# Optimization experiments

Hardware: AMD Instinct MI355X
Metric: run time of the kernel (lower is better)

The kernel has to match this reference:

```python
import jax, jax.numpy as jnp
import numpy as np

N_T, N_Y, N_X = 9, 256, 256
DIM_AE = 10
N_B = 16


def _conv(x, w):
    # Conv2d 3x3, stride 1, padding 1, no bias
    return jax.lax.conv_general_dilated(x, w, (1, 1), 'SAME',
                                        dimension_numbers=('NCHW', 'OIHW', 'NCHW'))


def _softplus10(x):
    # F.softplus(x, beta=10)
    return jax.nn.softplus(10.0 * x) / 10.0


def _derivs(u):
    # central finite differences with zero-Dirichlet boundary (dx=dy=1)
    up = jnp.pad(u, ((0, 0), (0, 0), (1, 1), (1, 1)))
    xp, xm = up[..., 2:, 1:-1], up[..., :-2, 1:-1]
    yp, ym = up[..., 1:-1, 2:], up[..., 1:-1, :-2]
    xpyp, xpym = up[..., 2:, 2:], up[..., 2:, :-2]
    xmyp, xmym = up[..., :-2, 2:], up[..., :-2, :-2]
    dx = 0.5 * (xp - xm)
    dy = 0.5 * (yp - ym)
    dxx = xp - 2.0 * u + xm
    dyy = yp - 2.0 * u + ym
    dxy = 0.25 * (xpyp - xpym - xmyp + xmym)
    return dx, dy, dxx, dyy, dxy


def _apply_A(u, kap, m1, m2, h11, h12, h21, h22):
    # SPDE operator: kappa^2 u + m.grad(u) - div(H grad u) (9-point stencil)
    dx, dy, dxx, dyy, dxy = _derivs(u)
    return kap ** 2 * u + m1 * dx + m2 * dy - (h11 * dxx + (h12 + h21) * dxy + h22 * dyy)


def setup_inputs() -> dict:
    key = jax.random.key(0)
    ks = jax.random.split(key, 4)
    x = jax.random.normal(ks[0], (N_B, N_T, N_Y, N_X), jnp.float32)
    kappa = jnp.zeros((1,), jnp.float32)   # overwritten by decoder (diff_only=False)
    m = jnp.zeros((1,), jnp.float32)       # overwritten by decoder
    H = jnp.zeros((N_B, 2, 2, N_Y * N_X, N_T), jnp.float32)  # overwritten by decoder
    def init_w(k, o, i):
        b = 1.0 / np.sqrt(i * 9)
        return jax.random.uniform(k, (o, i, 3, 3), jnp.float32, -b, b)
    w1 = init_w(ks[1], DIM_AE, N_T)
    w2 = init_w(ks[2], 2 * DIM_AE, DIM_AE)
    w3 = init_w(ks[3], 6 * N_T, 2 * DIM_AE)
    return {'x': x, 'kappa': kappa, 'm': m, 'H': H, 'w1': w1, 'w2': w2, 'w3': w3}


def reference(x, kappa, m, H, w1, w2, w3):
    n_b, n_t, n_y, n_x = x.shape
    N = n_y * n_x
    # ---- encoder ----
    p = _conv(jax.nn.relu(x), w1)
    p = _conv(jax.nn.relu(p), w2)
    p = _conv(p, w3)  # (b, 6*n_t, n_y, n_x)
    # ---- decoder ----
    kap = _softplus10(p[:, :n_t])                       # (b,t,y,x)
    md = jnp.stack([p[:, n_t:2 * n_t], p[:, 2 * n_t:3 * n_t]], axis=1)  # (b,2,t,y,x)
    gamma = _softplus10(p[:, 3 * n_t:4 * n_t])
    gflat = jnp.transpose(gamma, (0, 2, 3, 1)).reshape(n_b, N * n_t)    # (y,x,t) order
    vx = jnp.transpose(p[:, 4 * n_t:5 * n_t], (0, 2, 3, 1)).reshape(n_b, N * n_t)
    vy = jnp.transpose(p[:, 5 * n_t:6 * n_t], (0, 2, 3, 1)).reshape(n_b, N * n_t)
    vxy = jnp.stack([vx, vy], axis=2)                   # (b, K, 2)
    Hd = (jnp.einsum('ij,bk->bijk', jnp.eye(2, dtype=x.dtype), gflat)
          + jnp.einsum('bki,bkj->bijk', vxy, vxy))
    kap_d = kap.reshape(n_b, 1, N, n_t)        # literal reshapes as in original
    m_d = md.reshape(n_b, 2, N, n_t)
    H_d = Hd.reshape(n_b, 2, 2, N, n_t)
    # ---- per-timestep fields on (n_x, n_y) grid, node = ix*n_y + iy ----
    def to_grid(f):  # (b, N, t) -> (b, t, n_x, n_y)
        return jnp.transpose(f, (0, 2, 1)).reshape(n_b, n_t, n_x, n_y)
    kg = to_grid(kap_d[:, 0])
    m1g, m2g = to_grid(m_d[:, 0]), to_grid(m_d[:, 1])
    h11, h12 = to_grid(H_d[:, 0, 0]), to_grid(H_d[:, 0, 1])
    h21, h22 = to_grid(H_d[:, 1, 0]), to_grid(H_d[:, 1, 1])
    # ---- block-tridiagonal precision Q applied to x (never materialized) ----
    xg = jnp.transpose(x, (0, 1, 3, 2))  # (b,t,n_x,n_y), matches permute(0,2,1)
    M = lambda u: u + _apply_A(u, kg, m1g, m2g, h11, h12, h21, h22)  # I + dt*A, dt=1
    w = M(xg)   # M_t x_t
    v = M(w)    # M_t M_t x_t
    qx = jnp.concatenate([
        v[:, :1] - w[:, 1:2],
        -w[:, :-2] + v[:, 1:-1] + xg[:, 1:-1] - w[:, 2:],
        -w[:, -2:-1] + v[:, -1:],
    ], axis=1)
    x_out = jnp.sum(xg * qx, axis=(1, 2, 3))  # x^T Q x per batch, (b,)
    kappa_r = kap_d.reshape(n_b, 1, n_x, n_y, n_t)
    m_r = m_d.reshape(n_b, 2, n_x, n_y, n_t)
    H_r = H_d.reshape(n_b, 2, 2, n_x, n_y, n_t)
    return x_out, kappa_r, m_r, H_r
```

## Files before the change

kernel.cpp:

```cpp
#include <hip/hip_runtime.h>
#include <math.h>

#define NB 16
#define NT 9
#define PLANE 65536
#define KAP_B 589824
#define M_B   1179648
#define H_B   2359296

#define OUT_KAP 16
#define OUT_M   9437200
#define OUT_H   28311568

__device__ __forceinline__ float sp10(float x) {
  float z = 10.0f * x;
  return (fmaxf(z, 0.0f) + log1pf(__expf(-fabsf(z)))) * 0.1f;
}

__global__ __launch_bounds__(1024) void transpose_kernel(const float* __restrict__ x,
                                                         float* __restrict__ xg) {
  __shared__ float t_[32][33];
  const int plane = blockIdx.z;
  const float* src = x + (size_t)plane * PLANE;
  float* dst = xg + (size_t)plane * PLANE;
  const int x0 = blockIdx.x * 32, y0 = blockIdx.y * 32;
  t_[threadIdx.y][threadIdx.x] = src[(y0 + threadIdx.y) * 256 + x0 + threadIdx.x];
  __syncthreads();
  dst[(x0 + threadIdx.y) * 256 + (y0 + threadIdx.x)] = t_[threadIdx.x][threadIdx.y];
}

template <int IC, int OC, bool RELU_IN>
__global__ __launch_bounds__(256, 4) void conv2px(const float* __restrict__ in,
                                                  const float* __restrict__ wt,
                                                  float* __restrict__ out) {
  __shared__ float tile[IC][18][35];
  const int b = blockIdx.z;
  const int x0 = blockIdx.x * 32, y0 = blockIdx.y * 16;
  const int tx = threadIdx.x, ty = threadIdx.y;
  const int tid = ty * 16 + tx;
  const float* inb = in + (size_t)b * IC * PLANE;
  for (int idx = tid; idx < IC * 612; idx += 256) {
    int ic = idx / 612;
    int rem = idx - ic * 612;
    int r = rem / 34, c = rem - r * 34;
    int gy = y0 + r - 1, gx = x0 + c - 1;
    float v = 0.f;
    if (gy >= 0 && gy < 256 && gx >= 0 && gx < 256) {
      v = inb[ic * PLANE + gy * 256 + gx];
      if (RELU_IN) v = fmaxf(v, 0.f);
    }
    tile[ic][r][c] = v;
  }
  __syncthreads();
  float acc0[OC], acc1[OC];
#pragma unroll
  for (int oc = 0; oc < OC; ++oc) { acc0[oc] = 0.f; acc1[oc] = 0.f; }
  for (int ic = 0; ic < IC; ++ic) {
    float p[3][4];
#pragma unroll
    for (int r = 0; r < 3; ++r)
#pragma unroll
      for (int c = 0; c < 4; ++c) p[r][c] = tile[ic][ty + r][2 * tx + c];
#pragma unroll
    for (int oc = 0; oc < OC; ++oc) {
      const float* w9 = wt + (oc * IC + ic) * 9;
      acc0[oc] += p[0][0] * w9[0] + p[0][1] * w9[1] + p[0][2] * w9[2]
                + p[1][0] * w9[3] + p[1][1] * w9[4] + p[1][2] * w9[5]
                + p[2][0] * w9[6] + p[2][1] * w9[7] + p[2][2] * w9[8];
      acc1[oc] += p[0][1] * w9[0] + p[0][2] * w9[1] + p[0][3] * w9[2]
                + p[1][1] * w9[3] + p[1][2] * w9[4] + p[1][3] * w9[5]
                + p[2][1] * w9[6] + p[2][2] * w9[7] + p[2][3] * w9[8];
    }
  }
  float* outb = out + (size_t)b * OC * PLANE + (y0 + ty) * 256 + x0 + 2 * tx;
#pragma unroll
  for (int oc = 0; oc < OC; ++oc) {
    float2 v2 = make_float2(acc0[oc], acc1[oc]);
    *reinterpret_cast<float2*>(&outb[oc * PLANE]) = v2;
  }
}

__global__ __launch_bounds__(512, 4) void conv3_fused(const float* __restrict__ in,
                                                      const float* __restrict__ wt,
                                                      float* __restrict__ out_kap,
                                                      float* __restrict__ out_m,
                                                      float* __restrict__ out_H) {
  __shared__ float tile[20][18][35];
  const int b = blockIdx.z;
  const int x0 = blockIdx.x * 32, y0 = blockIdx.y * 16;
  const int tx = threadIdx.x, ty = threadIdx.y;
  const int h = __builtin_amdgcn_readfirstlane((int)threadIdx.z);
  const int tid = (int)threadIdx.z * 256 + ty * 16 + tx;
  const float* inb = in + (size_t)b * 20 * PLANE;
  for (int idx = tid; idx < 20 * 612; idx += 512) {
    int ic = idx / 612;
    int rem = idx - ic * 612;
    int r = rem / 34, c = rem - r * 34;
    int gy = y0 + r - 1, gx = x0 + c - 1;
    float v = 0.f;
    if (gy >= 0 && gy < 256 && gx >= 0 && gx < 256)
      v = inb[ic * PLANE + gy * 256 + gx];
    tile[ic][r][c] = v;
  }
  __syncthreads();
  float acc0[27], acc1[27];
#pragma unroll
  for (int oc = 0; oc < 27; ++oc) { acc0[oc] = 0.f; acc1[oc] = 0.f; }
  const float* wh = wt + (size_t)h * 27 * 20 * 9;
  for (int ic = 0; ic < 20; ++ic) {
    float p[3][4];
#pragma unroll
    for (int r = 0; r < 3; ++r)
#pragma unroll
      for (int c = 0; c < 4; ++c) p[r][c] = tile[ic][ty + r][2 * tx + c];
#pragma unroll
    for (int oc = 0; oc < 27; ++oc) {
      const float* w9 = wh + (oc * 20 + ic) * 9;
      acc0[oc] += p[0][0] * w9[0] + p[0][1] * w9[1] + p[0][2] * w9[2]
                + p[1][0] * w9[3] + p[1][1] * w9[4] + p[1][2] * w9[5]
                + p[2][0] * w9[6] + p[2][1] * w9[7] + p[2][2] * w9[8];
      acc1[oc] += p[0][1] * w9[0] + p[0][2] * w9[1] + p[0][3] * w9[2]
                + p[1][1] * w9[3] + p[1][2] * w9[4] + p[1][3] * w9[5]
                + p[2][1] * w9[6] + p[2][2] * w9[7] + p[2][3] * w9[8];
    }
  }
  const int n0 = (y0 + ty) * 256 + x0 + 2 * tx;
  if (h == 0) {
    float* kapb = out_kap + (size_t)b * KAP_B;
#pragma unroll
    for (int t = 0; t < 9; ++t) {
      float2 v2 = make_float2(sp10(acc0[t]), sp10(acc1[t]));
      *reinterpret_cast<float2*>(&kapb[t * PLANE + n0]) = v2;
    }
    float* mb = out_m + (size_t)b * M_B;
#pragma unroll
    for (int c = 0; c < 18; ++c) {
      float2 v2 = make_float2(acc0[9 + c], acc1[9 + c]);
      *reinterpret_cast<float2*>(&mb[c * PLANE + n0]) = v2;
    }
  } else {
    float* hb0 = out_H + (size_t)b * H_B + (size_t)n0 * 9;
#pragma unroll
    for (int t = 0; t < 9; ++t) {
      float g0 = sp10(acc0[t]), g1 = sp10(acc1[t]);
      float vx0 = acc0[9 + t], vy0 = acc0[18 + t];
      float vx1 = acc1[9 + t], vy1 = acc1[18 + t];
      hb0[t] = g0 + vx0 * vx0;
      hb0[KAP_B + t] = vx0 * vy0;
      hb0[2 * KAP_B + t] = vx0 * vy0;
      hb0[3 * KAP_B + t] = g0 + vy0 * vy0;
      hb0[9 + t] = g1 + vx1 * vx1;
      hb0[KAP_B + 9 + t] = vx1 * vy1;
      hb0[2 * KAP_B + 9 + t] = vx1 * vy1;
      hb0[3 * KAP_B + 9 + t] = g1 + vy1 * vy1;
    }
  }
}

template <bool FINAL>
__global__ __launch_bounds__(256) void m_kernel(const float* __restrict__ u_in,
                                                const float* __restrict__ dout,
                                                const float* __restrict__ xg,
                                                float* __restrict__ w_out,
                                                float* __restrict__ xsum) {
  __shared__ float u[9][18][18];
  __shared__ float red[256];
  const int b = blockIdx.z;
  const int X0 = blockIdx.y * 16;
  const int Y0 = blockIdx.x * 16;
  const int tx = threadIdx.x, ty = threadIdx.y;
  const int tid = ty * 16 + tx;
  const float* ub = u_in + (size_t)b * 9 * PLANE;
  for (int idx = tid; idx < 9 * 324; idx += 256) {
    int t = idx / 324;
    int rem = idx % 324;
    int r = rem / 18, c = rem % 18;
    int xx = X0 + r - 1, yy = Y0 + c - 1;
    float v = 0.f;
    if (xx >= 0 && xx < 256 && yy >= 0 && yy < 256)
      v = ub[t * PLANE + xx * 256 + yy];
    u[t][r][c] = v;
  }
  __syncthreads();
  const int xx = X0 + ty, yy = Y0 + tx;
  const int n = xx * 256 + yy;
  const float* kapb = dout + OUT_KAP + (size_t)b * KAP_B + (size_t)n * 9;
  const float* mb   = dout + OUT_M + (size_t)b * M_B + (size_t)n * 9;
  const float* hbb  = dout + OUT_H + (size_t)b * H_B + (size_t)n * 9;
  float csum = 0.f;
#pragma unroll
  for (int t = 0; t < 9; ++t) {
    float uc = u[t][ty + 1][tx + 1];
    float xp = u[t][ty + 2][tx + 1], xm = u[t][ty + 0][tx + 1];
    float yp = u[t][ty + 1][tx + 2], ym = u[t][ty + 1][tx + 0];
    float xpyp = u[t][ty + 2][tx + 2], xpym = u[t][ty + 2][tx + 0];
    float xmyp = u[t][ty + 0][tx + 2], xmym = u[t][ty + 0][tx + 0];
    float dx = 0.5f * (xp - xm), dy = 0.5f * (yp - ym);
    float dxx = xp - 2.f * uc + xm, dyy = yp - 2.f * uc + ym;
    float dxy = 0.25f * (xpyp - xpym - xmyp + xmym);
    float kap = kapb[t];
    float m1 = mb[t], m2 = mb[KAP_B + t];
    float h11 = hbb[t], h12 = hbb[KAP_B + t], h22 = hbb[3 * KAP_B + t];
    float r = uc + kap * kap * uc + m1 * dx + m2 * dy
            - (h11 * dxx + 2.f * h12 * dxy + h22 * dyy);
    if (!FINAL) {
      w_out[((size_t)(b * 9 + t)) * PLANE + n] = r;
    } else {
      float xgv = xg[((size_t)(b * 9 + t)) * PLANE + n];
      float q = r;
      if (t > 0) q -= u[t - 1][ty + 1][tx + 1];
      if (t < 8) q -= u[t + 1][ty + 1][tx + 1];
      if (t > 0 && t < 8) q += xgv;
      csum += xgv * q;
    }
  }
  if (FINAL) {
    red[tid] = csum;
    __syncthreads();
    for (int s = 128; s > 0; s >>= 1) {
      if (tid < s) red[tid] += red[tid + s];
      __syncthreads();
    }
    if (tid == 0) atomicAdd(xsum + b, red[0]);
  }
}

extern "C" void kernel_launch(void* const* d_in, const int* in_sizes, int n_in,
                              void* d_out, int out_size, void* d_ws, size_t ws_size,
                              hipStream_t stream) {
  const float* x  = (const float*)d_in[0];
  const float* w1 = (const float*)d_in[4];
  const float* w2 = (const float*)d_in[5];
  const float* w3 = (const float*)d_in[6];
  float* out = (float*)d_out;
  float* ws = (float*)d_ws;

  float* xg = ws;
  float* p1 = ws + 9437184;
  float* p2 = ws + 19922944;
  float* wbuf = ws + 9437184;

  hipMemsetAsync(d_out, 0, 16 * sizeof(float), stream);

  transpose_kernel<<<dim3(8, 8, NB * NT), dim3(32, 32), 0, stream>>>(x, xg);
  conv2px<9, 10, true><<<dim3(8, 16, NB), dim3(16, 16), 0, stream>>>(x, w1, p1);
  conv2px<10, 20, true><<<dim3(8, 16, NB), dim3(16, 16), 0, stream>>>(p1, w2, p2);
  conv3_fused<<<dim3(8, 16, NB), dim3(16, 16, 2), 0, stream>>>(p2, w3,
                                                               out + OUT_KAP, out + OUT_M, out + OUT_H);
  m_kernel<false><<<dim3(16, 16, NB), dim3(16, 16), 0, stream>>>(xg, out, nullptr, wbuf, nullptr);
  m_kernel<true><<<dim3(16, 16, NB), dim3(16, 16), 0, stream>>>(wbuf, out, xg, nullptr, out);
}
```

Baseline: 1.240 ms.

## Fuse two operator applications into one halo-recompute kernel and shrink conv3 tile

The two m_kernel passes become a single kernel that loads a 2-wide halo of x, computes w = M x on an 18x18 region in shared memory (recomputing the halo), then applies M again and reduces. This removes the global write and reread of the intermediate w and one launch, at the cost of redundant halo computation and extra coefficient loads. conv3_fused now stages input channels in two halves of 10 so the shared tile is smaller, and raises the occupancy hint to 6. Its H-field stores are also regrouped by component.

```diff
diff --git a/kernel.cpp b/kernel.cpp
--- a/kernel.cpp
+++ b/kernel.cpp
@@ -80,48 +80,51 @@
   }
 }
 
-__global__ __launch_bounds__(512, 4) void conv3_fused(const float* __restrict__ in,
+__global__ __launch_bounds__(512, 6) void conv3_fused(const float* __restrict__ in,
                                                       const float* __restrict__ wt,
                                                       float* __restrict__ out_kap,
                                                       float* __restrict__ out_m,
                                                       float* __restrict__ out_H) {
-  __shared__ float tile[20][18][35];
+  __shared__ float tile[10][18][35];
   const int b = blockIdx.z;
   const int x0 = blockIdx.x * 32, y0 = blockIdx.y * 16;
   const int tx = threadIdx.x, ty = threadIdx.y;
   const int h = __builtin_amdgcn_readfirstlane((int)threadIdx.z);
   const int tid = (int)threadIdx.z * 256 + ty * 16 + tx;
   const float* inb = in + (size_t)b * 20 * PLANE;
-  for (int idx = tid; idx < 20 * 612; idx += 512) {
-    int ic = idx / 612;
-    int rem = idx - ic * 612;
-    int r = rem / 34, c = rem - r * 34;
-    int gy = y0 + r - 1, gx = x0 + c - 1;
-    float v = 0.f;
-    if (gy >= 0 && gy < 256 && gx >= 0 && gx < 256)
-      v = inb[ic * PLANE + gy * 256 + gx];
-    tile[ic][r][c] = v;
-  }
-  __syncthreads();
   float acc0[27], acc1[27];
 #pragma unroll
   for (int oc = 0; oc < 27; ++oc) { acc0[oc] = 0.f; acc1[oc] = 0.f; }
   const float* wh = wt + (size_t)h * 27 * 20 * 9;
-  for (int ic = 0; ic < 20; ++ic) {
-    float p[3][4];
-#pragma unroll
-    for (int r = 0; r < 3; ++r)
-#pragma unroll
-      for (int c = 0; c < 4; ++c) p[r][c] = tile[ic][ty + r][2 * tx + c];
-#pragma unroll
-    for (int oc = 0; oc < 27; ++oc) {
-      const float* w9 = wh + (oc * 20 + ic) * 9;
-      acc0[oc] += p[0][0] * w9[0] + p[0][1] * w9[1] + p[0][2] * w9[2]
-                + p[1][0] * w9[3] + p[1][1] * w9[4] + p[1][2] * w9[5]
-                + p[2][0] * w9[6] + p[2][1] * w9[7] + p[2][2] * w9[8];
-      acc1[oc] += p[0][1] * w9[0] + p[0][2] * w9[1] + p[0][3] * w9[2]
-                + p[1][1] * w9[3] + p[1][2] * w9[4] + p[1][3] * w9[5]
-                + p[2][1] * w9[6] + p[2][2] * w9[7] + p[2][3] * w9[8];
+  for (int cc = 0; cc < 2; ++cc) {
+    if (cc) __syncthreads();
+    for (int idx = tid; idx < 10 * 612; idx += 512) {
+      int ic = idx / 612;
+      int rem = idx - ic * 612;
+      int r = rem / 34, c = rem - r * 34;
+      int gy = y0 + r - 1, gx = x0 + c - 1;
+      float v = 0.f;
+      if (gy >= 0 && gy < 256 && gx >= 0 && gx < 256)
+        v = inb[(cc * 10 + ic) * PLANE + gy * 256 + gx];
+      tile[ic][r][c] = v;
+    }
+    __syncthreads();
+    for (int ic = 0; ic < 10; ++ic) {
+      float p[3][4];
+#pragma unroll
+      for (int r = 0; r < 3; ++r)
+#pragma unroll
+        for (int c = 0; c < 4; ++c) p[r][c] = tile[ic][ty + r][2 * tx + c];
+#pragma unroll
+      for (int oc = 0; oc < 27; ++oc) {
+        const float* w9 = wh + (oc * 20 + cc * 10 + ic) * 9;
+        acc0[oc] += p[0][0] * w9[0] + p[0][1] * w9[1] + p[0][2] * w9[2]
+                  + p[1][0] * w9[3] + p[1][1] * w9[4] + p[1][2] * w9[5]
+                  + p[2][0] * w9[6] + p[2][1] * w9[7] + p[2][2] * w9[8];
+        acc1[oc] += p[0][1] * w9[0] + p[0][2] * w9[1] + p[0][3] * w9[2]
+                  + p[1][1] * w9[3] + p[1][2] * w9[4] + p[1][3] * w9[5]
+                  + p[2][1] * w9[6] + p[2][2] * w9[7] + p[2][3] * w9[8];
+      }
     }
   }
   const int n0 = (y0 + ty) * 256 + x0 + 2 * tx;
@@ -139,90 +142,116 @@
       *reinterpret_cast<float2*>(&mb[c * PLANE + n0]) = v2;
     }
   } else {
-    float* hb0 = out_H + (size_t)b * H_B + (size_t)n0 * 9;
-#pragma unroll
-    for (int t = 0; t < 9; ++t) {
-      float g0 = sp10(acc0[t]), g1 = sp10(acc1[t]);
-      float vx0 = acc0[9 + t], vy0 = acc0[18 + t];
-      float vx1 = acc1[9 + t], vy1 = acc1[18 + t];
-      hb0[t] = g0 + vx0 * vx0;
-      hb0[KAP_B + t] = vx0 * vy0;
-      hb0[2 * KAP_B + t] = vx0 * vy0;
-      hb0[3 * KAP_B + t] = g0 + vy0 * vy0;
-      hb0[9 + t] = g1 + vx1 * vx1;
-      hb0[KAP_B + 9 + t] = vx1 * vy1;
-      hb0[2 * KAP_B + 9 + t] = vx1 * vy1;
-      hb0[3 * KAP_B + 9 + t] = g1 + vy1 * vy1;
-    }
-  }
-}
-
-template <bool FINAL>
-__global__ __launch_bounds__(256) void m_kernel(const float* __restrict__ u_in,
-                                                const float* __restrict__ dout,
-                                                const float* __restrict__ xg,
-                                                float* __restrict__ w_out,
-                                                float* __restrict__ xsum) {
-  __shared__ float u[9][18][18];
+    float sg0[9], sg1[9];
+#pragma unroll
+    for (int t = 0; t < 9; ++t) { sg0[t] = sp10(acc0[t]); sg1[t] = sp10(acc1[t]); }
+    float* hb = out_H + (size_t)b * H_B + (size_t)n0 * 9;
+#pragma unroll
+    for (int t = 0; t < 9; ++t) hb[t] = sg0[t] + acc0[9 + t] * acc0[9 + t];
+#pragma unroll
+    for (int t = 0; t < 9; ++t) hb[9 + t] = sg1[t] + acc1[9 + t] * acc1[9 + t];
+#pragma unroll
+    for (int t = 0; t < 9; ++t) hb[KAP_B + t] = acc0[9 + t] * acc0[18 + t];
+#pragma unroll
+    for (int t = 0; t < 9; ++t) hb[KAP_B + 9 + t] = acc1[9 + t] * acc1[18 + t];
+#pragma unroll
+    for (int t = 0; t < 9; ++t) hb[2 * KAP_B + t] = acc0[9 + t] * acc0[18 + t];
+#pragma unroll
+    for (int t = 0; t < 9; ++t) hb[2 * KAP_B + 9 + t] = acc1[9 + t] * acc1[18 + t];
+#pragma unroll
+    for (int t = 0; t < 9; ++t) hb[3 * KAP_B + t] = sg0[t] + acc0[18 + t] * acc0[18 + t];
+#pragma unroll
+    for (int t = 0; t < 9; ++t) hb[3 * KAP_B + 9 + t] = sg1[t] + acc1[18 + t] * acc1[18 + t];
+  }
+}
+
+__global__ __launch_bounds__(256) void m_fused(const float* __restrict__ xgp,
+                                               const float* __restrict__ dout,
+                                               float* __restrict__ xsum) {
+  __shared__ float ux[9][20][21];
+  __shared__ float wsd[9][18][19];
   __shared__ float red[256];
   const int b = blockIdx.z;
   const int X0 = blockIdx.y * 16;
   const int Y0 = blockIdx.x * 16;
   const int tx = threadIdx.x, ty = threadIdx.y;
   const int tid = ty * 16 + tx;
-  const float* ub = u_in + (size_t)b * 9 * PLANE;
-  for (int idx = tid; idx < 9 * 324; idx += 256) {
-    int t = idx / 324;
-    int rem = idx % 324;
-    int r = rem / 18, c = rem % 18;
-    int xx = X0 + r - 1, yy = Y0 + c - 1;
+  const float* ub = xgp + (size_t)b * 9 * PLANE;
+  const float* kap_base = dout + OUT_KAP + (size_t)b * KAP_B;
+  const float* m_base   = dout + OUT_M + (size_t)b * M_B;
+  const float* h_base   = dout + OUT_H + (size_t)b * H_B;
+
+  for (int idx = tid; idx < 9 * 400; idx += 256) {
+    int t = idx / 400;
+    int rem = idx - t * 400;
+    int r = rem / 20, c = rem - r * 20;
+    int xx = X0 + r - 2, yy = Y0 + c - 2;
     float v = 0.f;
     if (xx >= 0 && xx < 256 && yy >= 0 && yy < 256)
       v = ub[t * PLANE + xx * 256 + yy];
-    u[t][r][c] = v;
-  }
-  __syncthreads();
+    ux[t][r][c] = v;
+  }
+  __syncthreads();
+
+  for (int idx = tid; idx < 9 * 324; idx += 256) {
+    int t = idx / 324;
+    int rem = idx - t * 324;
+    int r = rem / 18, c = rem - r * 18;
+    int xx = X0 + r - 1, yy = Y0 + c - 1;
+    float rw = 0.f;
+    if (xx >= 0 && xx < 256 && yy >= 0 && yy < 256) {
+      int n = xx * 256 + yy;
+      float uc = ux[t][r + 1][c + 1];
+      float xp = ux[t][r + 2][c + 1], xm = ux[t][r + 0][c + 1];
+      float yp = ux[t][r + 1][c + 2], ym = ux[t][r + 1][c + 0];
+      float xpyp = ux[t][r + 2][c + 2], xpym = ux[t][r + 2][c + 0];
+      float xmyp = ux[t][r + 0][c + 2], xmym = ux[t][r + 0][c + 0];
+      float dx = 0.5f * (xp - xm), dy = 0.5f * (yp - ym);
+      float dxx = xp - 2.f * uc + xm, dyy = yp - 2.f * uc + ym;
+      float dxy = 0.25f * (xpyp - xpym - xmyp + xmym);
+      size_t n9 = (size_t)n * 9 + t;
+      float kap = kap_base[n9];
+      float m1 = m_base[n9], m2 = m_base[KAP_B + n9];
+      float h11 = h_base[n9], h12 = h_base[KAP_B + n9], h22 = h_base[3 * (size_t)KAP_B + n9];
+      rw = uc + kap * kap * uc + m1 * dx + m2 * dy
+         - (h11 * dxx + 2.f * h12 * dxy + h22 * dyy);
+    }
+    wsd[t][r][c] = rw;
+  }
+  __syncthreads();
+
   const int xx = X0 + ty, yy = Y0 + tx;
-  const int n = xx * 256 + yy;
-  const float* kapb = dout + OUT_KAP + (size_t)b * KAP_B + (size_t)n * 9;
-  const float* mb   = dout + OUT_M + (size_t)b * M_B + (size_t)n * 9;
-  const float* hbb  = dout + OUT_H + (size_t)b * H_B + (size_t)n * 9;
+  const size_t n9 = ((size_t)(xx * 256 + yy)) * 9;
   float csum = 0.f;
 #pragma unroll
   for (int t = 0; t < 9; ++t) {
-    float uc = u[t][ty + 1][tx + 1];
-    float xp = u[t][ty + 2][tx + 1], xm = u[t][ty + 0][tx + 1];
-    float yp = u[t][ty + 1][tx + 2], ym = u[t][ty + 1][tx + 0];
-    float xpyp = u[t][ty + 2][tx + 2], xpym = u[t][ty + 2][tx + 0];
-    float xmyp = u[t][ty + 0][tx + 2], xmym = u[t][ty + 0][tx + 0];
+    float wc = wsd[t][ty + 1][tx + 1];
+    float xp = wsd[t][ty + 2][tx + 1], xm = wsd[t][ty + 0][tx + 1];
+    float yp = wsd[t][ty + 1][tx + 2], ym = wsd[t][ty + 1][tx + 0];
+    float xpyp = wsd[t][ty + 2][tx + 2], xpym = wsd[t][ty + 2][tx + 0];
+    float xmyp = wsd[t][ty + 0][tx + 2], xmym = wsd[t][ty + 0][tx + 0];
     float dx = 0.5f * (xp - xm), dy = 0.5f * (yp - ym);
-    float dxx = xp - 2.f * uc + xm, dyy = yp - 2.f * uc + ym;
+    float dxx = xp - 2.f * wc + xm, dyy = yp - 2.f * wc + ym;
     float dxy = 0.25f * (xpyp - xpym - xmyp + xmym);
-    float kap = kapb[t];
-    float m1 = mb[t], m2 = mb[KAP_B + t];
-    float h11 = hbb[t], h12 = hbb[KAP_B + t], h22 = hbb[3 * KAP_B + t];
-    float r = uc + kap * kap * uc + m1 * dx + m2 * dy
-            - (h11 * dxx + 2.f * h12 * dxy + h22 * dyy);
-    if (!FINAL) {
-      w_out[((size_t)(b * 9 + t)) * PLANE + n] = r;
-    } else {
-      float xgv = xg[((size_t)(b * 9 + t)) * PLANE + n];
-      float q = r;
-      if (t > 0) q -= u[t - 1][ty + 1][tx + 1];
-      if (t < 8) q -= u[t + 1][ty + 1][tx + 1];
-      if (t > 0 && t < 8) q += xgv;
-      csum += xgv * q;
-    }
-  }
-  if (FINAL) {
-    red[tid] = csum;
+    float kap = kap_base[n9 + t];
+    float m1 = m_base[n9 + t], m2 = m_base[KAP_B + n9 + t];
+    float h11 = h_base[n9 + t], h12 = h_base[KAP_B + n9 + t], h22 = h_base[3 * (size_t)KAP_B + n9 + t];
+    float rv = wc + kap * kap * wc + m1 * dx + m2 * dy
+             - (h11 * dxx + 2.f * h12 * dxy + h22 * dyy);
+    float xgv = ux[t][ty + 2][tx + 2];
+    float q = rv;
+    if (t > 0) q -= wsd[t - 1][ty + 1][tx + 1];
+    if (t < 8) q -= wsd[t + 1][ty + 1][tx + 1];
+    if (t > 0 && t < 8) q += xgv;
+    csum += xgv * q;
+  }
+  red[tid] = csum;
+  __syncthreads();
+  for (int s = 128; s > 0; s >>= 1) {
+    if (tid < s) red[tid] += red[tid + s];
     __syncthreads();
-    for (int s = 128; s > 0; s >>= 1) {
-      if (tid < s) red[tid] += red[tid + s];
-      __syncthreads();
-    }
-    if (tid == 0) atomicAdd(xsum + b, red[0]);
-  }
+  }
+  if (tid == 0) atomicAdd(xsum + b, red[0]);
 }
 
 extern "C" void kernel_launch(void* const* d_in, const int* in_sizes, int n_in,
@@ -238,7 +267,6 @@
   float* xg = ws;
   float* p1 = ws + 9437184;
   float* p2 = ws + 19922944;
-  float* wbuf = ws + 9437184;
 
   hipMemsetAsync(d_out, 0, 16 * sizeof(float), stream);
 
@@ -247,6 +275,5 @@
   conv2px<10, 20, true><<<dim3(8, 16, NB), dim3(16, 16), 0, stream>>>(p1, w2, p2);
   conv3_fused<<<dim3(8, 16, NB), dim3(16, 16, 2), 0, stream>>>(p2, w3,
                                                                out + OUT_KAP, out + OUT_M, out + OUT_H);
-  m_kernel<false><<<dim3(16, 16, NB), dim3(16, 16), 0, stream>>>(xg, out, nullptr, wbuf, nullptr);
-  m_kernel<true><<<dim3(16, 16, NB), dim3(16, 16), 0, stream>>>(wbuf, out, xg, nullptr, out);
-}
+  m_fused<<<dim3(16, 16, NB), dim3(16, 16), 0, stream>>>(xg, out, out);
+}
```

Measured after the change: 1.384 ms. 11.6% more time.

## Split conv3 output channels across four thread groups to cut register pressure

Applied to the files above, without the earlier changes.

The fused third convolution now uses four z-groups per block instead of two, each computing a smaller slice of the 54 output channels (14/13/15/12). This cuts the accumulator arrays per thread, and the launch bound is raised to allow more waves per SIMD. To keep 512 threads per block, the spatial tile is halved to 8 rows, which raises halo reload overhead in shared memory. The H epilogue is split by timestep range, with stores grouped by output plane.

```diff
diff --git a/kernel.cpp b/kernel.cpp
--- a/kernel.cpp
+++ b/kernel.cpp
@@ -80,21 +80,72 @@
   }
 }
 
-__global__ __launch_bounds__(512, 4) void conv3_fused(const float* __restrict__ in,
+template <int NCH, int B0, int N0, int B1, int N1, int B2>
+__device__ __forceinline__ void slice_conv(const float (&tile)[20][10][35],
+                                           const float* __restrict__ wt,
+                                           int tx, int ty,
+                                           float (&a0)[NCH], float (&a1)[NCH]) {
+#pragma unroll
+  for (int j = 0; j < NCH; ++j) { a0[j] = 0.f; a1[j] = 0.f; }
+  for (int ic = 0; ic < 20; ++ic) {
+    float p[3][4];
+#pragma unroll
+    for (int r = 0; r < 3; ++r)
+#pragma unroll
+      for (int c = 0; c < 4; ++c) p[r][c] = tile[ic][ty + r][2 * tx + c];
+#pragma unroll
+    for (int j = 0; j < NCH; ++j) {
+      const int gc = (j < N0) ? (B0 + j) : (j < N0 + N1) ? (B1 + j - N0) : (B2 + j - N0 - N1);
+      const float* w9 = wt + (gc * 20 + ic) * 9;
+      a0[j] += p[0][0] * w9[0] + p[0][1] * w9[1] + p[0][2] * w9[2]
+             + p[1][0] * w9[3] + p[1][1] * w9[4] + p[1][2] * w9[5]
+             + p[2][0] * w9[6] + p[2][1] * w9[7] + p[2][2] * w9[8];
+      a1[j] += p[0][1] * w9[0] + p[0][2] * w9[1] + p[0][3] * w9[2]
+             + p[1][1] * w9[3] + p[1][2] * w9[4] + p[1][3] * w9[5]
+             + p[2][1] * w9[6] + p[2][2] * w9[7] + p[2][3] * w9[8];
+    }
+  }
+}
+
+template <int T0, int NTT>
+__device__ __forceinline__ void h_epilogue(const float (&a0)[3 * NTT], const float (&a1)[3 * NTT],
+                                           float* __restrict__ hb) {
+  float sg0[NTT], sg1[NTT];
+#pragma unroll
+  for (int j = 0; j < NTT; ++j) { sg0[j] = sp10(a0[j]); sg1[j] = sp10(a1[j]); }
+#pragma unroll
+  for (int j = 0; j < NTT; ++j) hb[T0 + j] = sg0[j] + a0[NTT + j] * a0[NTT + j];
+#pragma unroll
+  for (int j = 0; j < NTT; ++j) hb[9 + T0 + j] = sg1[j] + a1[NTT + j] * a1[NTT + j];
+#pragma unroll
+  for (int j = 0; j < NTT; ++j) hb[KAP_B + T0 + j] = a0[NTT + j] * a0[2 * NTT + j];
+#pragma unroll
+  for (int j = 0; j < NTT; ++j) hb[KAP_B + 9 + T0 + j] = a1[NTT + j] * a1[2 * NTT + j];
+#pragma unroll
+  for (int j = 0; j < NTT; ++j) hb[2 * KAP_B + T0 + j] = a0[NTT + j] * a0[2 * NTT + j];
+#pragma unroll
+  for (int j = 0; j < NTT; ++j) hb[2 * KAP_B + 9 + T0 + j] = a1[NTT + j] * a1[2 * NTT + j];
+#pragma unroll
+  for (int j = 0; j < NTT; ++j) hb[3 * KAP_B + T0 + j] = sg0[j] + a0[2 * NTT + j] * a0[2 * NTT + j];
+#pragma unroll
+  for (int j = 0; j < NTT; ++j) hb[3 * KAP_B + 9 + T0 + j] = sg1[j] + a1[2 * NTT + j] * a1[2 * NTT + j];
+}
+
+__global__ __launch_bounds__(512, 6) void conv3_fused(const float* __restrict__ in,
                                                       const float* __restrict__ wt,
                                                       float* __restrict__ out_kap,
                                                       float* __restrict__ out_m,
                                                       float* __restrict__ out_H) {
-  __shared__ float tile[20][18][35];
+  __shared__ float tile[20][10][35];
   const int b = blockIdx.z;
-  const int x0 = blockIdx.x * 32, y0 = blockIdx.y * 16;
+  const int x0 = blockIdx.x * 32, y0 = blockIdx.y * 8;
   const int tx = threadIdx.x, ty = threadIdx.y;
   const int h = __builtin_amdgcn_readfirstlane((int)threadIdx.z);
-  const int tid = (int)threadIdx.z * 256 + ty * 16 + tx;
+  const int tid = (int)threadIdx.z * 128 + ty * 16 + tx;
   const float* inb = in + (size_t)b * 20 * PLANE;
-  for (int idx = tid; idx < 20 * 612; idx += 512) {
-    int ic = idx / 612;
-    int rem = idx - ic * 612;
+  for (int idx = tid; idx < 20 * 340; idx += 512) {
+    int ic = idx / 340;
+    int rem = idx - ic * 340;
     int r = rem / 34, c = rem - r * 34;
     int gy = y0 + r - 1, gx = x0 + c - 1;
     float v = 0.f;
@@ -103,57 +154,33 @@
     tile[ic][r][c] = v;
   }
   __syncthreads();
-  float acc0[27], acc1[27];
-#pragma unroll
-  for (int oc = 0; oc < 27; ++oc) { acc0[oc] = 0.f; acc1[oc] = 0.f; }
-  const float* wh = wt + (size_t)h * 27 * 20 * 9;
-  for (int ic = 0; ic < 20; ++ic) {
-    float p[3][4];
-#pragma unroll
-    for (int r = 0; r < 3; ++r)
-#pragma unroll
-      for (int c = 0; c < 4; ++c) p[r][c] = tile[ic][ty + r][2 * tx + c];
-#pragma unroll
-    for (int oc = 0; oc < 27; ++oc) {
-      const float* w9 = wh + (oc * 20 + ic) * 9;
-      acc0[oc] += p[0][0] * w9[0] + p[0][1] * w9[1] + p[0][2] * w9[2]
-                + p[1][0] * w9[3] + p[1][1] * w9[4] + p[1][2] * w9[5]
-                + p[2][0] * w9[6] + p[2][1] * w9[7] + p[2][2] * w9[8];
-      acc1[oc] += p[0][1] * w9[0] + p[0][2] * w9[1] + p[0][3] * w9[2]
-                + p[1][1] * w9[3] + p[1][2] * w9[4] + p[1][3] * w9[5]
-                + p[2][1] * w9[6] + p[2][2] * w9[7] + p[2][3] * w9[8];
-    }
-  }
   const int n0 = (y0 + ty) * 256 + x0 + 2 * tx;
   if (h == 0) {
+    float a0[14], a1[14];
+    slice_conv<14, 0, 14, 0, 0, 0>(tile, wt, tx, ty, a0, a1);
     float* kapb = out_kap + (size_t)b * KAP_B;
 #pragma unroll
-    for (int t = 0; t < 9; ++t) {
-      float2 v2 = make_float2(sp10(acc0[t]), sp10(acc1[t]));
-      *reinterpret_cast<float2*>(&kapb[t * PLANE + n0]) = v2;
-    }
+    for (int t = 0; t < 9; ++t)
+      *reinterpret_cast<float2*>(&kapb[t * PLANE + n0]) = make_float2(sp10(a0[t]), sp10(a1[t]));
     float* mb = out_m + (size_t)b * M_B;
 #pragma unroll
-    for (int c = 0; c < 18; ++c) {
-      float2 v2 = make_float2(acc0[9 + c], acc1[9 + c]);
-      *reinterpret_cast<float2*>(&mb[c * PLANE + n0]) = v2;
-    }
+    for (int k = 0; k < 5; ++k)
+      *reinterpret_cast<float2*>(&mb[k * PLANE + n0]) = make_float2(a0[9 + k], a1[9 + k]);
+  } else if (h == 1) {
+    float a0[13], a1[13];
+    slice_conv<13, 14, 13, 0, 0, 0>(tile, wt, tx, ty, a0, a1);
+    float* mb = out_m + (size_t)b * M_B;
+#pragma unroll
+    for (int k = 0; k < 13; ++k)
+      *reinterpret_cast<float2*>(&mb[(5 + k) * PLANE + n0]) = make_float2(a0[k], a1[k]);
+  } else if (h == 2) {
+    float a0[15], a1[15];
+    slice_conv<15, 27, 5, 36, 5, 45>(tile, wt, tx, ty, a0, a1);
+    h_epilogue<0, 5>(a0, a1, out_H + (size_t)b * H_B + (size_t)n0 * 9);
   } else {
-    float* hb0 = out_H + (size_t)b * H_B + (size_t)n0 * 9;
-#pragma unroll
-    for (int t = 0; t < 9; ++t) {
-      float g0 = sp10(acc0[t]), g1 = sp10(acc1[t]);
-      float vx0 = acc0[9 + t], vy0 = acc0[18 + t];
-      float vx1 = acc1[9 + t], vy1 = acc1[18 + t];
-      hb0[t] = g0 + vx0 * vx0;
-      hb0[KAP_B + t] = vx0 * vy0;
-      hb0[2 * KAP_B + t] = vx0 * vy0;
-      hb0[3 * KAP_B + t] = g0 + vy0 * vy0;
-      hb0[9 + t] = g1 + vx1 * vx1;
-      hb0[KAP_B + 9 + t] = vx1 * vy1;
-      hb0[2 * KAP_B + 9 + t] = vx1 * vy1;
-      hb0[3 * KAP_B + 9 + t] = g1 + vy1 * vy1;
-    }
+    float a0[12], a1[12];
+    slice_conv<12, 32, 4, 41, 4, 50>(tile, wt, tx, ty, a0, a1);
+    h_epilogue<5, 4>(a0, a1, out_H + (size_t)b * H_B + (size_t)n0 * 9);
   }
 }
 
@@ -245,8 +272,8 @@
   transpose_kernel<<<dim3(8, 8, NB * NT), dim3(32, 32), 0, stream>>>(x, xg);
   conv2px<9, 10, true><<<dim3(8, 16, NB), dim3(16, 16), 0, stream>>>(x, w1, p1);
   conv2px<10, 20, true><<<dim3(8, 16, NB), dim3(16, 16), 0, stream>>>(p1, w2, p2);
-  conv3_fused<<<dim3(8, 16, NB), dim3(16, 16, 2), 0, stream>>>(p2, w3,
-                                                               out + OUT_KAP, out + OUT_M, out + OUT_H);
+  conv3_fused<<<dim3(8, 32, NB), dim3(16, 8, 4), 0, stream>>>(p2, w3,
+                                                              out + OUT_KAP, out + OUT_M, out + OUT_H);
   m_kernel<false><<<dim3(16, 16, NB), dim3(16, 16), 0, stream>>>(xg, out, nullptr, wbuf, nullptr);
   m_kernel<true><<<dim3(16, 16, NB), dim3(16, 16), 0, stream>>>(wbuf, out, xg, nullptr, out);
 }
```

New measurement: 1.214 ms. 1.02x faster.
